# Performance work log

Measured on AMD Instinct MI355X. Metric: run time of the kernel, lower is better.

Reference implementation:

```python
import math
import jax, jax.numpy as jnp
import numpy as np

B, N = 8, 2048
IN_DIM = COND_DIM = ATTN_DIM = OUT_DIM = 128
NUM_HEADS = 4
DH = ATTN_DIM // NUM_HEADS  # 32


def setup_inputs() -> dict:
    key = jax.random.key(0)
    ks = jax.random.split(key, 10)
    s_in = 1.0 / math.sqrt(IN_DIM)
    s_cd = 1.0 / math.sqrt(COND_DIM)
    return {
        "x": jax.random.normal(ks[0], (B, N, IN_DIM), jnp.float32),
        "cond": jax.random.normal(ks[1], (B, N, COND_DIM), jnp.float32),
        "flags": jnp.ones((B, N, 1), jnp.float32),
        "attention_mask": jax.random.normal(ks[2], (B, N, N), jnp.float32),
        # Linear params (stored [in, out]; torch Linear is x @ W.T + b)
        "Wq": jax.random.uniform(ks[3], (IN_DIM, ATTN_DIM), jnp.float32, -s_in, s_in),
        "bq": jax.random.uniform(ks[4], (ATTN_DIM,), jnp.float32, -s_in, s_in),
        "Wk": jax.random.uniform(ks[5], (COND_DIM, ATTN_DIM), jnp.float32, -s_cd, s_cd),
        "bk": jax.random.uniform(ks[6], (ATTN_DIM,), jnp.float32, -s_cd, s_cd),
        "Wv": jax.random.uniform(ks[7], (COND_DIM, OUT_DIM), jnp.float32, -s_cd, s_cd),
        "bv": jax.random.uniform(ks[8], (OUT_DIM,), jnp.float32, -s_cd, s_cd),
    }


def reference(x, cond, flags, attention_mask, Wq, bq, Wk, bk, Wv, bv):
    # flags is accepted but unused, matching the original forward.
    b, n, _ = x.shape
    Q = (x @ Wq + bq).reshape(b, n, NUM_HEADS, DH)     # channel-split heads
    K = (cond @ Wk + bk).reshape(b, n, NUM_HEADS, DH)
    V = cond @ Wv + bv                                 # [B, N, OUT_DIM]
    # per-head scores, scaled by sqrt(out_dim) as in the original
    S = jnp.einsum("bnhd,bmhd->hbnm", Q, K) / math.sqrt(OUT_DIM)
    A = jnp.tanh(attention_mask[None] + S)             # tanh activation, not softmax
    A = A.mean(axis=0)                                 # head-mean -> [B, N, N]
    return jnp.einsum("bnm,bmd->bnd", A, V)
```

## Files before the change

### kernel.cpp

```cpp
#include <hip/hip_runtime.h>
#include <hip/hip_bf16.h>

typedef __attribute__((ext_vector_type(4))) float f32x4;
typedef __attribute__((ext_vector_type(8))) short bf16x8;

#define MFMA16(A, B, C) __builtin_amdgcn_mfma_f32_16x16x32_bf16(A, B, C, 0, 0, 0)

#define C2 2.8853900817779268f
#define QS (2.8853900817779268f / 11.313708498984761f)

__device__ __forceinline__ unsigned cvtpk_bf16(float lo, float hi) {
    unsigned r;
    asm("v_cvt_pk_bf16_f32 %0, %1, %2" : "=v"(r) : "v"(lo), "v"(hi));
    return r;
}

__device__ __forceinline__ bf16x8 pack8(float4 a, float4 b) {
    union { unsigned u[4]; bf16x8 v; } u;
    u.u[0] = cvtpk_bf16(a.x, a.y);
    u.u[1] = cvtpk_bf16(a.z, a.w);
    u.u[2] = cvtpk_bf16(b.x, b.y);
    u.u[3] = cvtpk_bf16(b.z, b.w);
    return u.v;
}

__device__ __forceinline__ void gload_lds16(const void* g, void* l) {
    __builtin_amdgcn_global_load_lds(
        (const __attribute__((address_space(1))) unsigned int*)g,
        (__attribute__((address_space(3))) unsigned int*)l, 16, 0, 0);
}

__global__ void prep_weights(const float* __restrict__ Wq, const float* __restrict__ bq,
                             const float* __restrict__ Wk, const float* __restrict__ bk,
                             const float* __restrict__ Wv, const float* __restrict__ bv,
                             __hip_bfloat16* __restrict__ Wqt, __hip_bfloat16* __restrict__ Wkt,
                             __hip_bfloat16* __restrict__ Wvt, float* __restrict__ bias) {
    int i = blockIdx.x * 256 + threadIdx.x;
    int k = i >> 7, o = i & 127;
    Wqt[o * 128 + k] = __float2bfloat16(Wq[i] * QS);
    Wkt[o * 128 + k] = __float2bfloat16(Wk[i]);
    Wvt[o * 128 + k] = __float2bfloat16(Wv[i] * 0.25f);
    if (i < 128) {
        bias[i]       = bq[i] * QS;
        bias[128 + i] = bk[i];
        bias[256 + i] = bv[i] * 0.25f;
    }
}

__global__ __launch_bounds__(256) void proj_qkv(
        const float* __restrict__ x, const float* __restrict__ cond,
        const __hip_bfloat16* __restrict__ Wqt, const __hip_bfloat16* __restrict__ Wkt,
        const __hip_bfloat16* __restrict__ Wvt, const float* __restrict__ bias,
        __hip_bfloat16* __restrict__ Qo, __hip_bfloat16* __restrict__ Ko,
        __hip_bfloat16* __restrict__ Vt) {
    const int lane = threadIdx.x & 63, wv = threadIdx.x >> 6;
    const int l15 = lane & 15, g = lane >> 4;
    const int row0 = blockIdx.x * 64 + wv * 16;

    f32x4 qa[8], ka[8], va[8];
#pragma unroll
    for (int ot = 0; ot < 8; ++ot) {
        float b0 = bias[16 * ot + l15];
        float b1 = bias[128 + 16 * ot + l15];
        float b2 = bias[256 + 16 * ot + l15];
        qa[ot] = (f32x4){b0, b0, b0, b0};
        ka[ot] = (f32x4){b1, b1, b1, b1};
        va[ot] = (f32x4){b2, b2, b2, b2};
    }

    const float* xp = x    + (size_t)(row0 + l15) * 128 + 8 * g;
    const float* cp = cond + (size_t)(row0 + l15) * 128 + 8 * g;
#pragma unroll
    for (int kk = 0; kk < 4; ++kk) {
        float4 x0 = *(const float4*)(xp + 32 * kk);
        float4 x1 = *(const float4*)(xp + 32 * kk + 4);
        float4 c0 = *(const float4*)(cp + 32 * kk);
        float4 c1 = *(const float4*)(cp + 32 * kk + 4);
        bf16x8 xa = pack8(x0, x1);
        bf16x8 ca = pack8(c0, c1);
#pragma unroll
        for (int ot = 0; ot < 8; ++ot) {
            const int wo = (16 * ot + l15) * 128 + 32 * kk + 8 * g;
            qa[ot] = MFMA16(xa, *(const bf16x8*)(Wqt + wo), qa[ot]);
            ka[ot] = MFMA16(ca, *(const bf16x8*)(Wkt + wo), ka[ot]);
            va[ot] = MFMA16(ca, *(const bf16x8*)(Wvt + wo), va[ot]);
        }
    }

#pragma unroll
    for (int ot = 0; ot < 8; ++ot)
#pragma unroll
        for (int r = 0; r < 4; ++r) {
            size_t idx = (size_t)(row0 + 4 * g + r) * 128 + 16 * ot + l15;
            Qo[idx] = __float2bfloat16(qa[ot][r]);
            Ko[idx] = __float2bfloat16(ka[ot][r]);
        }
    const int bb = row0 >> 11, nn = (row0 & 2047) + 4 * g;
#pragma unroll
    for (int ot = 0; ot < 8; ++ot) {
        uint2 pr;
        pr.x = cvtpk_bf16(va[ot][0], va[ot][1]);
        pr.y = cvtpk_bf16(va[ot][2], va[ot][3]);
        *(uint2*)((unsigned short*)Vt + ((size_t)bb * 128 + 16 * ot + l15) * 2048 + nn) = pr;
    }
}

__global__ __launch_bounds__(512) void attn_main(
        const __hip_bfloat16* __restrict__ Q, const __hip_bfloat16* __restrict__ K,
        const __hip_bfloat16* __restrict__ Vt, const float* __restrict__ mask,
        float* __restrict__ out) {
    __shared__ __align__(16) char Kl[2][16384];
    __shared__ __align__(16) char Vl[2][16384];
    __shared__ __align__(16) char Al[64 * 144];

    const int lane = threadIdx.x & 63, w = threadIdx.x >> 6;
    const int l15 = lane & 15, g = lane >> 4;
    const int qw = w & 3, mw = w >> 2, dw = mw;
    const int b  = blockIdx.x & 7;
    const int r2 = blockIdx.x >> 3;
    const int qt = r2 & 31;
    const int mh = r2 >> 5;
    const int n0 = qt * 64;
    const int mh0 = mh * 1024;

    const __hip_bfloat16* Qb = Q + ((size_t)b * 2048 + n0 + qw * 16) * 128;
    const char* Kg = (const char*)(K + (size_t)b * 2048 * 128);
    const char* Vg = (const char*)(Vt + (size_t)b * 128 * 2048);
    const float* mrow = mask + ((size_t)b * 2048 + n0 + qw * 16 + l15) * 2048
                        + mh0 + mw * 32 + 4 * g;

    bf16x8 qf[4];
#pragma unroll
    for (int h = 0; h < 4; ++h)
        qf[h] = *(const bf16x8*)(Qb + l15 * 128 + 32 * h + 8 * g);

    f32x4 oacc[4];
#pragma unroll
    for (int dtl = 0; dtl < 4; ++dtl) oacc[dtl] = (f32x4){0.f, 0.f, 0.f, 0.f};
    const f32x4 zero = (f32x4){0.f, 0.f, 0.f, 0.f};

    auto STAGE = [&](int m0g, int bi) {
#pragma unroll
        for (int i = 0; i < 2; ++i) {
            const int t = w * 2 + i;
            const int o = t * 1024 + lane * 16;
            const int kr = o >> 8, kc = o & 255;
            gload_lds16(Kg + (size_t)(m0g + kr) * 256 + (kc ^ ((kr & 7) << 4)),
                        &Kl[bi][t * 1024]);
            const int vr = o >> 7, vc = o & 127;
            gload_lds16(Vg + (size_t)vr * 4096 + (size_t)m0g * 2 + (vc ^ ((vr & 7) << 4)),
                        &Vl[bi][t * 1024]);
        }
    };

    STAGE(mh0, 0);
    f32x4 mkc0 = *(const f32x4*)(mrow);
    f32x4 mkc1 = *(const f32x4*)(mrow + 16);
    asm volatile("s_waitcnt vmcnt(0)" ::: "memory");
    __builtin_amdgcn_s_barrier();

#pragma unroll 2
    for (int c = 0; c < 16; ++c) {
        const int bi = c & 1;
        const int m0g = mh0 + c * 64;
        if (c < 15) STAGE(m0g + 64, bi ^ 1);
        f32x4 mkn0, mkn1;
        if (c < 15) {
            mkn0 = *(const f32x4*)(mrow + (c + 1) * 64);
            mkn1 = *(const f32x4*)(mrow + (c + 1) * 64 + 16);
        }

#pragma unroll
        for (int st = 0; st < 2; ++st) {
            const int mr = mw * 32 + st * 16 + l15;
            const char* kb = &Kl[bi][mr * 256];
            const int sw = (mr & 7) << 4;
            f32x4 s0 = MFMA16(*(const bf16x8*)(kb + ((g * 16) ^ sw)),       qf[0], zero);
            f32x4 s1 = MFMA16(*(const bf16x8*)(kb + ((64 + g * 16) ^ sw)),  qf[1], zero);
            f32x4 s2 = MFMA16(*(const bf16x8*)(kb + ((128 + g * 16) ^ sw)), qf[2], zero);
            f32x4 s3 = MFMA16(*(const bf16x8*)(kb + ((192 + g * 16) ^ sw)), qf[3], zero);
            const f32x4 mk = st ? mkc1 : mkc0;
            float acd[4];
#pragma unroll
            for (int r = 0; r < 4; ++r) {
                float m2 = mk[r] * C2;
                float e0 = __builtin_amdgcn_exp2f(m2 + s0[r]);
                float e1 = __builtin_amdgcn_exp2f(m2 + s1[r]);
                float e2 = __builtin_amdgcn_exp2f(m2 + s2[r]);
                float e3 = __builtin_amdgcn_exp2f(m2 + s3[r]);
                float rs = __builtin_amdgcn_rcpf(1.f + e0) + __builtin_amdgcn_rcpf(1.f + e1)
                         + __builtin_amdgcn_rcpf(1.f + e2) + __builtin_amdgcn_rcpf(1.f + e3);
                acd[r] = 4.f - 2.f * rs;
            }
            uint2 pk;
            pk.x = cvtpk_bf16(acd[0], acd[1]);
            pk.y = cvtpk_bf16(acd[2], acd[3]);
            *(uint2*)(Al + (qw * 16 + l15) * 144 + (mw * 32 + st * 16 + 4 * g) * 2) = pk;
        }

        asm volatile("s_waitcnt lgkmcnt(0)" ::: "memory");
        __builtin_amdgcn_s_barrier();

#pragma unroll
        for (int ks = 0; ks < 2; ++ks) {
            bf16x8 af = *(const bf16x8*)(Al + (qw * 16 + l15) * 144 + (ks * 32 + 8 * g) * 2);
#pragma unroll
            for (int dtl = 0; dtl < 4; ++dtl) {
                const int dr = dw * 64 + dtl * 16 + l15;
                bf16x8 vf = *(const bf16x8*)(
                    &Vl[bi][dr * 128 + ((ks * 64 + g * 16) ^ ((dr & 7) << 4))]);
                oacc[dtl] = MFMA16(af, vf, oacc[dtl]);
            }
        }

        asm volatile("s_waitcnt vmcnt(0)" ::: "memory");
        __builtin_amdgcn_s_barrier();

        mkc0 = mkn0;
        mkc1 = mkn1;
    }

    float* ob = out + ((size_t)b * 2048 + n0 + qw * 16) * 128 + dw * 64;
#pragma unroll
    for (int dtl = 0; dtl < 4; ++dtl)
#pragma unroll
        for (int r = 0; r < 4; ++r)
            unsafeAtomicAdd(&ob[(size_t)(4 * g + r) * 128 + dtl * 16 + l15], oacc[dtl][r]);
}

extern "C" void kernel_launch(void* const* d_in, const int* in_sizes, int n_in,
                              void* d_out, int out_size, void* d_ws, size_t ws_size,
                              hipStream_t stream) {
    const float* x    = (const float*)d_in[0];
    const float* cond = (const float*)d_in[1];
    const float* mask = (const float*)d_in[3];
    const float* Wq = (const float*)d_in[4];
    const float* bq = (const float*)d_in[5];
    const float* Wk = (const float*)d_in[6];
    const float* bk = (const float*)d_in[7];
    const float* Wv = (const float*)d_in[8];
    const float* bv = (const float*)d_in[9];
    float* out = (float*)d_out;

    char* ws = (char*)d_ws;
    __hip_bfloat16* Qo  = (__hip_bfloat16*)(ws);
    __hip_bfloat16* Ko  = (__hip_bfloat16*)(ws + (4  << 20));
    __hip_bfloat16* Vt  = (__hip_bfloat16*)(ws + (8  << 20));
    __hip_bfloat16* Wqt = (__hip_bfloat16*)(ws + (12 << 20));
    __hip_bfloat16* Wkt = (__hip_bfloat16*)(ws + (12 << 20) + 32768);
    __hip_bfloat16* Wvt = (__hip_bfloat16*)(ws + (12 << 20) + 65536);
    float*          bias = (float*)(ws + (12 << 20) + 98304);

    hipMemsetAsync(d_out, 0, (size_t)out_size * sizeof(float), stream);

    prep_weights<<<64, 256, 0, stream>>>(Wq, bq, Wk, bk, Wv, bv, Wqt, Wkt, Wvt, bias);
    proj_qkv<<<256, 256, 0, stream>>>(x, cond, Wqt, Wkt, Wvt, bias, Qo, Ko, Vt);
    attn_main<<<512, 512, 0, stream>>>(Qo, Ko, Vt, mask, out);
}
```

Before: 87.08 us.

## Keep attention tile in registers via ds_bpermute instead of LDS round-trip

Removes the shared-memory A tile and the mid-iteration barrier. Each wave now keeps its own m-slice of the tanh scores in registers, rearranges them into an MFMA operand with ds_bpermute, and computes the partial A·V over all 128 output columns for that slice. Partial sums from the two m-halves are then combined through the existing atomic adds. K and V swizzles change to suit the new access patterns. The cost is double the output accumulators and twice as many atomics per block.

```diff
diff --git a/kernel.cpp b/kernel.cpp
--- a/kernel.cpp
+++ b/kernel.cpp
@@ -111,11 +111,10 @@
         float* __restrict__ out) {
     __shared__ __align__(16) char Kl[2][16384];
     __shared__ __align__(16) char Vl[2][16384];
-    __shared__ __align__(16) char Al[64 * 144];
 
     const int lane = threadIdx.x & 63, w = threadIdx.x >> 6;
     const int l15 = lane & 15, g = lane >> 4;
-    const int qw = w & 3, mw = w >> 2, dw = mw;
+    const int qw = w & 3, mw = w >> 2;
     const int b  = blockIdx.x & 7;
     const int r2 = blockIdx.x >> 3;
     const int qt = r2 & 31;
@@ -134,10 +133,14 @@
     for (int h = 0; h < 4; ++h)
         qf[h] = *(const bf16x8*)(Qb + l15 * 128 + 32 * h + 8 * g);
 
-    f32x4 oacc[4];
-#pragma unroll
-    for (int dtl = 0; dtl < 4; ++dtl) oacc[dtl] = (f32x4){0.f, 0.f, 0.f, 0.f};
+    f32x4 oacc[8];
+#pragma unroll
+    for (int dt = 0; dt < 8; ++dt) oacc[dt] = (f32x4){0.f, 0.f, 0.f, 0.f};
     const f32x4 zero = (f32x4){0.f, 0.f, 0.f, 0.f};
+
+    const int idxA = (l15 + 16 * ((2 * g) & 3)) * 4;
+    const int idxB = (l15 + 16 * ((2 * g + 1) & 3)) * 4;
+    const bool lowg = (g < 2);
 
     auto STAGE = [&](int m0g, int bi) {
 #pragma unroll
@@ -145,10 +148,10 @@
             const int t = w * 2 + i;
             const int o = t * 1024 + lane * 16;
             const int kr = o >> 8, kc = o & 255;
-            gload_lds16(Kg + (size_t)(m0g + kr) * 256 + (kc ^ ((kr & 7) << 4)),
+            gload_lds16(Kg + (size_t)(m0g + kr) * 256 + (kc ^ ((kr & 7) << 5)),
                         &Kl[bi][t * 1024]);
             const int vr = o >> 7, vc = o & 127;
-            gload_lds16(Vg + (size_t)vr * 4096 + (size_t)m0g * 2 + (vc ^ ((vr & 7) << 4)),
+            gload_lds16(Vg + (size_t)vr * 4096 + (size_t)m0g * 2 + (vc ^ ((vr & 3) << 5)),
                         &Vl[bi][t * 1024]);
         }
     };
@@ -162,19 +165,19 @@
 #pragma unroll 2
     for (int c = 0; c < 16; ++c) {
         const int bi = c & 1;
-        const int m0g = mh0 + c * 64;
-        if (c < 15) STAGE(m0g + 64, bi ^ 1);
+        if (c < 15) STAGE(mh0 + (c + 1) * 64, bi ^ 1);
         f32x4 mkn0, mkn1;
         if (c < 15) {
             mkn0 = *(const f32x4*)(mrow + (c + 1) * 64);
             mkn1 = *(const f32x4*)(mrow + (c + 1) * 64 + 16);
         }
 
+        unsigned tx[2], ty[2];
 #pragma unroll
         for (int st = 0; st < 2; ++st) {
             const int mr = mw * 32 + st * 16 + l15;
             const char* kb = &Kl[bi][mr * 256];
-            const int sw = (mr & 7) << 4;
+            const int sw = (mr & 7) << 5;
             f32x4 s0 = MFMA16(*(const bf16x8*)(kb + ((g * 16) ^ sw)),       qf[0], zero);
             f32x4 s1 = MFMA16(*(const bf16x8*)(kb + ((64 + g * 16) ^ sw)),  qf[1], zero);
             f32x4 s2 = MFMA16(*(const bf16x8*)(kb + ((128 + g * 16) ^ sw)), qf[2], zero);
@@ -192,25 +195,32 @@
                          + __builtin_amdgcn_rcpf(1.f + e2) + __builtin_amdgcn_rcpf(1.f + e3);
                 acd[r] = 4.f - 2.f * rs;
             }
-            uint2 pk;
-            pk.x = cvtpk_bf16(acd[0], acd[1]);
-            pk.y = cvtpk_bf16(acd[2], acd[3]);
-            *(uint2*)(Al + (qw * 16 + l15) * 144 + (mw * 32 + st * 16 + 4 * g) * 2) = pk;
-        }
-
-        asm volatile("s_waitcnt lgkmcnt(0)" ::: "memory");
-        __builtin_amdgcn_s_barrier();
-
-#pragma unroll
-        for (int ks = 0; ks < 2; ++ks) {
-            bf16x8 af = *(const bf16x8*)(Al + (qw * 16 + l15) * 144 + (ks * 32 + 8 * g) * 2);
-#pragma unroll
-            for (int dtl = 0; dtl < 4; ++dtl) {
-                const int dr = dw * 64 + dtl * 16 + l15;
-                bf16x8 vf = *(const bf16x8*)(
-                    &Vl[bi][dr * 128 + ((ks * 64 + g * 16) ^ ((dr & 7) << 4))]);
-                oacc[dtl] = MFMA16(af, vf, oacc[dtl]);
-            }
+            tx[st] = cvtpk_bf16(acd[0], acd[1]);
+            ty[st] = cvtpk_bf16(acd[2], acd[3]);
+        }
+
+        union { unsigned u[4]; bf16x8 v; } af;
+        {
+            unsigned a0 = __builtin_amdgcn_ds_bpermute(idxA, (int)tx[0]);
+            unsigned b0 = __builtin_amdgcn_ds_bpermute(idxA, (int)tx[1]);
+            unsigned a1 = __builtin_amdgcn_ds_bpermute(idxA, (int)ty[0]);
+            unsigned b1 = __builtin_amdgcn_ds_bpermute(idxA, (int)ty[1]);
+            unsigned a2 = __builtin_amdgcn_ds_bpermute(idxB, (int)tx[0]);
+            unsigned b2 = __builtin_amdgcn_ds_bpermute(idxB, (int)tx[1]);
+            unsigned a3 = __builtin_amdgcn_ds_bpermute(idxB, (int)ty[0]);
+            unsigned b3 = __builtin_amdgcn_ds_bpermute(idxB, (int)ty[1]);
+            af.u[0] = lowg ? a0 : b0;
+            af.u[1] = lowg ? a1 : b1;
+            af.u[2] = lowg ? a2 : b2;
+            af.u[3] = lowg ? a3 : b3;
+        }
+
+#pragma unroll
+        for (int dt = 0; dt < 8; ++dt) {
+            const int dr = dt * 16 + l15;
+            bf16x8 vf = *(const bf16x8*)(
+                &Vl[bi][dr * 128 + ((mw * 64 + g * 16) ^ ((dr & 3) << 5))]);
+            oacc[dt] = MFMA16(vf, af.v, oacc[dt]);
         }
 
         asm volatile("s_waitcnt vmcnt(0)" ::: "memory");
@@ -220,12 +230,12 @@
         mkc1 = mkn1;
     }
 
-    float* ob = out + ((size_t)b * 2048 + n0 + qw * 16) * 128 + dw * 64;
-#pragma unroll
-    for (int dtl = 0; dtl < 4; ++dtl)
+    float* ob = out + ((size_t)b * 2048 + n0 + qw * 16 + l15) * 128;
+#pragma unroll
+    for (int dt = 0; dt < 8; ++dt)
 #pragma unroll
         for (int r = 0; r < 4; ++r)
-            unsafeAtomicAdd(&ob[(size_t)(4 * g + r) * 128 + dtl * 16 + l15], oacc[dtl][r]);
+            unsafeAtomicAdd(&ob[dt * 16 + 4 * g + r], oacc[dt][r]);
 }
 
 extern "C" void kernel_launch(void* const* d_in, const int* in_sizes, int n_in,
```

After: 174.3 us. 2x slower.
